# Kernel tuning notes

Measured on AMD Instinct MI355X. Metric: run time of the kernel, lower is better.

## Reference

```python
import jax, jax.numpy as jnp
import numpy as np

# Static module config (from init_kwargs)
IMG_H, IMG_W = 256, 704
NX, NY, NZ = 200, 200, 4
VOX = (0.5, 0.5, 1.5)
B, NCAM, C, HF, WF = 2, 6, 256, 64, 176
STRIDE = -(-IMG_W // WF)  # math.ceil(704/176) = 4
OUT_C = 80
BN_EPS = 1e-5


def _camera_mats():
    """Realistic lidar2image = K @ extrinsic for 6 surround cameras."""
    K = np.array([[300., 0., 352., 0.],
                  [0., 300., 128., 0.],
                  [0., 0., 1., 0.],
                  [0., 0., 0., 1.]])
    mats = []
    for a in np.linspace(0.0, 2 * np.pi, NCAM, endpoint=False):
        fwd = np.array([np.cos(a), np.sin(a), 0.0])   # camera z (forward)
        right = np.array([np.sin(a), -np.cos(a), 0.0])  # camera x
        down = np.array([0.0, 0.0, -1.0])             # camera y
        R = np.stack([right, down, fwd])
        E = np.eye(4)
        E[:3, :3] = R
        mats.append(K @ E)
    return np.stack(mats).astype(np.float32)  # [NCAM,4,4]


def setup_inputs() -> dict:
    key = jax.random.key(0)
    k1, k2, k3 = jax.random.split(key, 3)
    mlvl_feats = jax.random.normal(k1, (B, NCAM, C, HF, WF), jnp.float32)
    points = jax.random.uniform(k2, (B, NZ, NX, NY), jnp.float32)  # per-voxel weights
    lidar2image = jnp.asarray(np.tile(_camera_mats()[None], (B, 1, 1, 1)))
    img_aug_matrix = jnp.tile(jnp.eye(4, dtype=jnp.float32)[None, None], (B, NCAM, 1, 1))
    lidar_aug_matrix = jnp.tile(jnp.eye(4, dtype=jnp.float32)[None], (B, 1, 1))
    conv_w = jax.random.normal(k3, (OUT_C, C), jnp.float32) * 0.02
    conv_b = jnp.zeros((OUT_C,), jnp.float32)
    bn_gamma = jnp.ones((OUT_C,), jnp.float32)
    bn_beta = jnp.zeros((OUT_C,), jnp.float32)
    return dict(mlvl_feats=mlvl_feats, points=points, lidar2image=lidar2image,
                img_aug_matrix=img_aug_matrix, lidar_aug_matrix=lidar_aug_matrix,
                conv_w=conv_w, conv_b=conv_b, bn_gamma=bn_gamma, bn_beta=bn_beta)


def _voxel_grid():
    # get_points(): voxel-center world coordinates, [3, NX*NY*NZ]
    idx = jnp.stack(jnp.meshgrid(jnp.arange(NX), jnp.arange(NY), jnp.arange(NZ), indexing='ij'))
    vs = jnp.array(VOX, jnp.float32)
    origin = jnp.array([0.0, 0.0, -1.0], jnp.float32) - jnp.array([NX, NY, NZ], jnp.float32) / 2.0 * vs
    pts = idx.astype(jnp.float32) * vs.reshape(3, 1, 1, 1) + origin.reshape(3, 1, 1, 1)
    return pts.reshape(3, -1)


def _backproject(feat, l2i, img_aug, lidar_aug, grid):
    # feat [NCAM,C,HF,WF]; l2i/img_aug [NCAM,4,4]; lidar_aug [4,4]; grid [3,V]
    V = grid.shape[1]
    lt = lidar_aug[:3, 3]
    lr = lidar_aug[:3, :3]
    img_t = img_aug[:, :, 3]                 # [NCAM,4]
    img_r = img_aug.at[:, :, 3].set(0.0)     # zero last column
    proj = (img_r @ l2i)[:, :3, :]           # [NCAM,3,4]
    pts = lr.T @ (grid - lt[:, None])        # inverse lidar aug
    pts_h = jnp.concatenate([pts, jnp.ones((1, V), grid.dtype)], axis=0)  # [4,V]
    p2i = jnp.einsum('nij,jv->niv', proj, pts_h)  # [NCAM,3,V]
    z = p2i[:, 2]
    u = p2i[:, 0] / z + img_t[:, 0:1]
    v = p2i[:, 1] / z + img_t[:, 1:2]
    uf = jnp.round(u / STRIDE).astype(jnp.int32)
    vf = jnp.round(v / STRIDE).astype(jnp.int32)
    valid = (uf >= 0) & (vf >= 0) & (uf < WF) & (vf < HF) & (z > 0)
    uc = jnp.clip(uf, 0, WF - 1)
    vc = jnp.clip(vf, 0, HF - 1)
    vol = jnp.zeros((C, V), feat.dtype)
    # later cameras overwrite earlier ones (matches torch per-image assignment loop)
    for n in range(NCAM):
        vol = jnp.where(valid[n][None, :], feat[n][:, vc[n], uc[n]], vol)
    return vol.reshape(C, NX, NY, NZ)


def reference(mlvl_feats, points, lidar2image, img_aug_matrix, lidar_aug_matrix,
              conv_w, conv_b, bn_gamma, bn_beta):
    grid = _voxel_grid()
    volumes = jax.vmap(_backproject, in_axes=(0, 0, 0, 0, None))(
        mlvl_feats, lidar2image, img_aug_matrix, lidar_aug_matrix, grid)  # [B,C,NX,NY,NZ]
    w = jnp.transpose(points, (0, 2, 3, 1))[:, None]  # [B,1,NX,NY,NZ]
    bev = (volumes * w).sum(-1)                       # weighted z-reduction -> [B,C,NX,NY]
    y = jnp.einsum('bchw,oc->bohw', bev, conv_w) + conv_b[None, :, None, None]
    mean = y.mean((0, 2, 3), keepdims=True)
    var = y.var((0, 2, 3), keepdims=True)
    y = (y - mean) * jax.lax.rsqrt(var + BN_EPS)
    y = y * bn_gamma[None, :, None, None] + bn_beta[None, :, None, None]
    return jax.nn.relu(y)
```

## Files before the change

### kernel.cpp

```cpp
#include <hip/hip_runtime.h>

#define B_ 2
#define NCAM_ 6
#define C_ 256
#define HF_ 64
#define WF_ 176
#define NX_ 200
#define NY_ 200
#define NZ_ 4
#define V_ (NX_*NY_*NZ_)
#define HW_ (HF_*WF_)
#define OUTC_ 80
#define NPOS_ (NX_*NY_)
#define NBLK3_ 1250

typedef unsigned short u16;
typedef unsigned int   u32;
typedef __attribute__((ext_vector_type(8))) short bf16x8;
typedef __attribute__((ext_vector_type(4))) float f32x4;
typedef __attribute__((ext_vector_type(2))) unsigned int u32x2;
typedef __attribute__((ext_vector_type(4))) unsigned int u32x4;

#define WS_PROJ 0
#define WS_IMGT 144
#define WS_SCALE 256
#define WS_SHIFT 336
#define WS_WB   2048
#define WS_PF   336384
#define WS_PART 5743104
#define WS_YBF  5943104

__device__ __forceinline__ u16 f2bf(float x) {
    u32 u = __float_as_uint(x);
    u32 r = (u + 0x7fffu + ((u >> 16) & 1u)) >> 16;
    return (u16)r;
}
__device__ __forceinline__ float bf2f(u16 v) {
    return __uint_as_float(((u32)v) << 16);
}

__global__ void k0_prep(const float* __restrict__ l2i,
                        const float* __restrict__ img_aug,
                        const float* __restrict__ conv_w,
                        float* __restrict__ ws)
{
    int t = threadIdx.x;
    if (t < B_*NCAM_*12) {
        int bn = t / 12;
        int e  = t % 12;
        int i = e >> 2, j = e & 3;
        const float* A = img_aug + bn*16;
        const float* L = l2i + bn*16;
        float acc = 0.f;
        #pragma unroll
        for (int k = 0; k < 4; ++k) {
            float a = (k < 3) ? A[i*4 + k] : 0.f;
            acc = fmaf(a, L[k*4 + j], acc);
        }
        ws[WS_PROJ + t] = acc;
    }
    if (t >= 192 && t < 192 + B_*NCAM_*2) {
        int s = t - 192;
        int bn = s >> 1, i = s & 1;
        ws[WS_IMGT + s] = img_aug[bn*16 + i*4 + 3];
    }
    u32* wbp = (u32*)(ws + WS_WB);
    for (int i = t; i < 8*5*64*4; i += 256) {
        int ks = i / 1280;
        int r  = i - ks*1280;
        int u  = r >> 8;
        int r2 = r & 255;
        int l  = r2 >> 2;
        int j  = r2 & 3;
        int la = l & 15, hi = l >> 4;
        int o  = u*16 + la;
        int cb = ks*32 + ((j >> 1) << 4) + hi*4 + ((j & 1) << 1);
        wbp[i] = (u32)f2bf(conv_w[o*C_ + cb]) | ((u32)f2bf(conv_w[o*C_ + cb + 1]) << 16);
    }
}

__global__ __launch_bounds__(256, 8) void k2_mfma(const float* __restrict__ feat,
                                                  const u32* __restrict__ wbp,
                                                  u16* __restrict__ pf)
{
    __shared__ float lds[2][32][64];
    const int bn  = blockIdx.y;
    const int x   = blockIdx.x;
    const int xsw = (x & 7)*22 + (x >> 3);
    const int hw0 = xsw*64;
    const int t   = threadIdx.x;
    const int wv  = t >> 6;
    const int l   = t & 63;
    const int la  = l & 15;
    const int hi  = l >> 4;

    const float* fb = feat + (size_t)bn*C_*HW_ + hw0;

#define STAGE(buf, c0) do { \
    _Pragma("unroll") for (int i_ = 0; i_ < 2; ++i_) { \
        int r0_ = i_*16 + wv*4; \
        const float* src_ = fb + (size_t)((c0) + r0_ + (l >> 4))*HW_ + (l & 15)*4; \
        __builtin_amdgcn_global_load_lds( \
            (const __attribute__((address_space(1))) unsigned int*)src_, \
            (__attribute__((address_space(3))) unsigned int*)&lds[buf][r0_][0], \
            16, 0, 0); \
    } \
} while (0)

    f32x4 acc[5] = {};
    STAGE(0, 0);
    for (int ks = 0; ks < 8; ++ks) {
        const int cur = ks & 1;
        __syncthreads();
        if (ks < 7) STAGE(cur ^ 1, (ks+1)*32);
        const int hwl = wv*16 + la;
        union { u32 u[4]; bf16x8 v; } Bf;
        #pragma unroll
        for (int j = 0; j < 4; ++j) {
            const int cb = ((j >> 1) << 4) + hi*4 + ((j & 1) << 1);
            Bf.u[j] = (u32)f2bf(lds[cur][cb][hwl]) |
                      ((u32)f2bf(lds[cur][cb+1][hwl]) << 16);
        }
        #pragma unroll
        for (int u = 0; u < 5; ++u) {
            union { u32x4 q; bf16x8 v; } A;
            A.q = *(const u32x4*)&wbp[((ks*5 + u)*64 + l)*4];
            acc[u] = __builtin_amdgcn_mfma_f32_16x16x32_bf16(A.v, Bf.v, acc[u], 0, 0, 0);
        }
    }
#undef STAGE

    __syncthreads();
    u16* yt = (u16*)lds;
    {
        const int hwl = wv*16 + la;
        #pragma unroll
        for (int u = 0; u < 5; ++u) {
            f32x4 a = acc[u];
            u32 p0 = (u32)f2bf(a.x) | ((u32)f2bf(a.y) << 16);
            u32 p1 = (u32)f2bf(a.z) | ((u32)f2bf(a.w) << 16);
            u32x2 pk; pk.x = p0; pk.y = p1;
            *(u32x2*)&yt[hwl*80 + u*16 + hi*4] = pk;
        }
    }
    __syncthreads();
    const u32x4* src128 = (const u32x4*)yt;
    u32x4* dst128 = (u32x4*)(pf + (size_t)(bn*HW_ + hw0)*80);
    #pragma unroll
    for (int i = 0; i < 3; ++i) {
        int k = t + i*256;
        if (k < 640) dst128[k] = src128[k];
    }
}

__global__ __launch_bounds__(320) void k3_gather(const float* __restrict__ ws,
                                                 const float* __restrict__ lidar_aug,
                                                 const float* __restrict__ points,
                                                 const u16* __restrict__ pf,
                                                 const float* __restrict__ conv_b,
                                                 u16* __restrict__ ybf,
                                                 float* __restrict__ part)
{
    __shared__ int   idx_s[256];
    __shared__ float w_s[256];
    __shared__ float y_s[OUTC_][65];
    const int wlin = blockIdx.y*625 + blockIdx.x;
    const int q = NBLK3_ >> 3, r = NBLK3_ & 7;
    const int xcd = wlin & 7, iw = wlin >> 3;
    const int wg = (xcd < r) ? xcd*(q+1) + iw : r*(q+1) + (xcd - r)*q + iw;
    const int b = wg / 625;
    const int tile = wg - b*625;
    int t = threadIdx.x;
    if (t < 256) {
        int izl = t >> 6, p = t & 63;
        w_s[izl*64 + p] = points[b*V_ + izl*NPOS_ + tile*64 + p];
        int v = tile*256 + t;
        int ixy = v >> 2;
        int iz  = v & 3;
        int ix = ixy / NY_;
        int iy = ixy - ix*NY_;
        float x = ix*0.5f - 50.f;
        float y = iy*0.5f - 50.f;
        float z = iz*1.5f - 4.f;
        const float* la = lidar_aug + b*16;
        float gx = x - la[3], gy = y - la[7], gz = z - la[11];
        float px = fmaf(la[8],  gz, fmaf(la[4], gy, fmaf(la[0], gx, 0.f)));
        float py = fmaf(la[9],  gz, fmaf(la[5], gy, fmaf(la[1], gx, 0.f)));
        float pz = fmaf(la[10], gz, fmaf(la[6], gy, fmaf(la[2], gx, 0.f)));
        int best = -1;
        #pragma unroll
        for (int n = 0; n < NCAM_; ++n) {
            const float* P = ws + WS_PROJ + (b*NCAM_ + n)*12;
            float t0 = fmaf(P[3], 1.f, fmaf(P[2],  pz, fmaf(P[1], py, fmaf(P[0], px, 0.f))));
            float t1 = fmaf(P[7], 1.f, fmaf(P[6],  pz, fmaf(P[5], py, fmaf(P[4], px, 0.f))));
            float t2 = fmaf(P[11],1.f, fmaf(P[10], pz, fmaf(P[9], py, fmaf(P[8], px, 0.f))));
            float u = t0/t2 + ws[WS_IMGT + (b*NCAM_+n)*2 + 0];
            float w = t1/t2 + ws[WS_IMGT + (b*NCAM_+n)*2 + 1];
            int uf = (int)rintf(u*0.25f);
            int vf = (int)rintf(w*0.25f);
            if (uf >= 0 && vf >= 0 && uf < WF_ && vf < HF_ && t2 > 0.f)
                best = n*HW_ + vf*WF_ + uf;
        }
        idx_s[t] = best;
    }
    __syncthreads();
    int og = (t % 10)*8;
    int pg = t / 10;
    float bb0 = conv_b[og],   bb1 = conv_b[og+1], bb2 = conv_b[og+2], bb3 = conv_b[og+3];
    float bb4 = conv_b[og+4], bb5 = conv_b[og+5], bb6 = conv_b[og+6], bb7 = conv_b[og+7];
    const u16* pfb = pf + (size_t)b*(NCAM_*HW_)*80;
    #pragma unroll
    for (int i = 0; i < 2; ++i) {
        int p = pg*2 + i;
        float a0 = bb0, a1 = bb1, a2 = bb2, a3 = bb3;
        float a4 = bb4, a5 = bb5, a6 = bb6, a7 = bb7;
        #pragma unroll
        for (int iz = 0; iz < 4; ++iz) {
            int g = idx_s[p*4 + iz];
            if (g >= 0) {
                u32x4 w4 = *(const u32x4*)&pfb[(size_t)g*80 + og];
                float wgt = w_s[iz*64 + p];
                a0 = fmaf(wgt, bf2f((u16)(w4.x & 0xffff)), a0);
                a1 = fmaf(wgt, bf2f((u16)(w4.x >> 16)),    a1);
                a2 = fmaf(wgt, bf2f((u16)(w4.y & 0xffff)), a2);
                a3 = fmaf(wgt, bf2f((u16)(w4.y >> 16)),    a3);
                a4 = fmaf(wgt, bf2f((u16)(w4.z & 0xffff)), a4);
                a5 = fmaf(wgt, bf2f((u16)(w4.z >> 16)),    a5);
                a6 = fmaf(wgt, bf2f((u16)(w4.w & 0xffff)), a6);
                a7 = fmaf(wgt, bf2f((u16)(w4.w >> 16)),    a7);
            }
        }
        y_s[og][p]   = a0; y_s[og+1][p] = a1;
        y_s[og+2][p] = a2; y_s[og+3][p] = a3;
        y_s[og+4][p] = a4; y_s[og+5][p] = a5;
        y_s[og+6][p] = a6; y_s[og+7][p] = a7;
    }
    __syncthreads();
    u16* yb = ybf + (size_t)b*OUTC_*NPOS_ + tile*64;
    for (int lq = t; lq < OUTC_*32; lq += 320) {
        int oo = lq >> 5, p2 = (lq & 31) << 1;
        u32 pk = (u32)f2bf(y_s[oo][p2]) | ((u32)f2bf(y_s[oo][p2+1]) << 16);
        *(u32*)&yb[(size_t)oo*NPOS_ + p2] = pk;
    }
    int oo = t >> 2, qq = t & 3;
    float s1 = 0.f, s2 = 0.f;
    #pragma unroll
    for (int i = 0; i < 16; ++i) {
        float v = y_s[oo][qq*16 + i];
        s1 += v; s2 += v*v;
    }
    s1 += __shfl_xor(s1, 1, 4); s2 += __shfl_xor(s2, 1, 4);
    s1 += __shfl_xor(s1, 2, 4); s2 += __shfl_xor(s2, 2, 4);
    if (qq == 0) {
        int bb = b*625 + tile;
        part[oo*NBLK3_ + bb] = s1;
        part[OUTC_*NBLK3_ + oo*NBLK3_ + bb] = s2;
    }
}

__global__ __launch_bounds__(256) void k4_final(const float* __restrict__ part,
                                                const float* __restrict__ gamma,
                                                const float* __restrict__ beta,
                                                float* __restrict__ ws)
{
    int o = blockIdx.x;
    int t = threadIdx.x;
    float s1 = 0.f, s2 = 0.f;
    for (int j = t; j < NBLK3_; j += 256) {
        s1 += part[o*NBLK3_ + j];
        s2 += part[OUTC_*NBLK3_ + o*NBLK3_ + j];
    }
    __shared__ float r1[256], r2[256];
    r1[t] = s1; r2[t] = s2;
    __syncthreads();
    for (int s = 128; s > 0; s >>= 1) {
        if (t < s) { r1[t] += r1[t+s]; r2[t] += r2[t+s]; }
        __syncthreads();
    }
    if (t == 0) {
        const float invN = 1.f/(float)(B_*NPOS_);
        float mean = r1[0]*invN;
        float var  = r2[0]*invN - mean*mean;
        float inv  = rsqrtf(var + 1e-5f);
        float sc   = gamma[o]*inv;
        ws[WS_SCALE + o] = sc;
        ws[WS_SHIFT + o] = beta[o] - mean*sc;
    }
}

__global__ __launch_bounds__(256) void k5_norm(const u32* __restrict__ ybf,
                                               const float* __restrict__ ws,
                                               float* __restrict__ out)
{
    int gid = blockIdx.x*256 + threadIdx.x;
    int f = gid*8;
    if (f >= B_*OUTC_*NPOS_) return;
    int o = (f / NPOS_) % OUTC_;
    float sc = ws[WS_SCALE + o], sh = ws[WS_SHIFT + o];
    u32x4 v = *(const u32x4*)&ybf[gid*4];
    float4 r0, r1;
    r0.x = fmaxf(fmaf(bf2f((u16)(v.x & 0xffff)), sc, sh), 0.f);
    r0.y = fmaxf(fmaf(bf2f((u16)(v.x >> 16)),    sc, sh), 0.f);
    r0.z = fmaxf(fmaf(bf2f((u16)(v.y & 0xffff)), sc, sh), 0.f);
    r0.w = fmaxf(fmaf(bf2f((u16)(v.y >> 16)),    sc, sh), 0.f);
    r1.x = fmaxf(fmaf(bf2f((u16)(v.z & 0xffff)), sc, sh), 0.f);
    r1.y = fmaxf(fmaf(bf2f((u16)(v.z >> 16)),    sc, sh), 0.f);
    r1.z = fmaxf(fmaf(bf2f((u16)(v.w & 0xffff)), sc, sh), 0.f);
    r1.w = fmaxf(fmaf(bf2f((u16)(v.w >> 16)),    sc, sh), 0.f);
    *(float4*)&out[f]     = r0;
    *(float4*)&out[f + 4] = r1;
}

extern "C" void kernel_launch(void* const* d_in, const int* in_sizes, int n_in,
                              void* d_out, int out_size, void* d_ws, size_t ws_size,
                              hipStream_t stream) {
    (void)in_sizes; (void)n_in; (void)out_size; (void)ws_size;
    const float* feat      = (const float*)d_in[0];
    const float* points    = (const float*)d_in[1];
    const float* l2i       = (const float*)d_in[2];
    const float* img_aug   = (const float*)d_in[3];
    const float* lidar_aug = (const float*)d_in[4];
    const float* conv_w    = (const float*)d_in[5];
    const float* conv_b    = (const float*)d_in[6];
    const float* gamma     = (const float*)d_in[7];
    const float* beta      = (const float*)d_in[8];
    float* out = (float*)d_out;
    float* wsf = (float*)d_ws;
    u32*   wbp = (u32*)(wsf + WS_WB);
    u16*   pf  = (u16*)(wsf + WS_PF);
    float* part = wsf + WS_PART;
    u16*   ybf = (u16*)(wsf + WS_YBF);

    hipLaunchKernelGGL(k0_prep, dim3(1), dim3(256), 0, stream, l2i, img_aug, conv_w, wsf);
    hipLaunchKernelGGL(k2_mfma, dim3(HW_/64, B_*NCAM_), dim3(256), 0, stream, feat, wbp, pf);
    hipLaunchKernelGGL(k3_gather, dim3(625, B_), dim3(320), 0, stream, wsf, lidar_aug, points, pf, conv_b, ybf, part);
    hipLaunchKernelGGL(k4_final, dim3(OUTC_), dim3(256), 0, stream, part, gamma, beta, wsf);
    hipLaunchKernelGGL(k5_norm, dim3((B_*OUTC_*NPOS_/8)/256 + 1, 1), dim3(256), 0, stream, (const u32*)ybf, wsf, out);
}
```

Before: 66.67 us.

## Skip projecting feature tiles never referenced by any voxel

Adds a pass that projects every voxel into every camera and, in an occupancy bitmap, marks which 64-pixel feature tiles are the last-camera hit. The MFMA channel-projection kernel then exits early for tiles no voxel uses, avoiding their feature loads and matrix work. This costs an extra kernel launch and the per-voxel projection maths, and it relies on the flag computation matching the gather kernel's indexing exactly.

```diff
diff --git a/kernel.cpp b/kernel.cpp
--- a/kernel.cpp
+++ b/kernel.cpp
@@ -25,6 +25,7 @@
 #define WS_IMGT 144
 #define WS_SCALE 256
 #define WS_SHIFT 336
+#define WS_FLG  1024
 #define WS_WB   2048
 #define WS_PF   336384
 #define WS_PART 5743104
@@ -64,6 +65,8 @@
         int bn = s >> 1, i = s & 1;
         ws[WS_IMGT + s] = img_aug[bn*16 + i*4 + 3];
     }
+    u32* flags = (u32*)(ws + WS_FLG);
+    if (t < 66) flags[t] = 0;
     u32* wbp = (u32*)(ws + WS_WB);
     for (int i = t; i < 8*5*64*4; i += 256) {
         int ks = i / 1280;
@@ -79,8 +82,52 @@
     }
 }
 
+__global__ __launch_bounds__(256) void k1_flags(const float* __restrict__ ws,
+                                                const float* __restrict__ lidar_aug,
+                                                u32* __restrict__ flags)
+{
+    __shared__ u32 fl[33];
+    const int wg = blockIdx.x;
+    const int b = wg / 625;
+    const int tile = wg - b*625;
+    const int t = threadIdx.x;
+    if (t < 33) fl[t] = 0;
+    __syncthreads();
+    int v = tile*256 + t;
+    int ixy = v >> 2;
+    int iz  = v & 3;
+    int ix = ixy / NY_;
+    int iy = ixy - ix*NY_;
+    float x = ix*0.5f - 50.f;
+    float y = iy*0.5f - 50.f;
+    float z = iz*1.5f - 4.f;
+    const float* la = lidar_aug + b*16;
+    float gx = x - la[3], gy = y - la[7], gz = z - la[11];
+    float px = fmaf(la[8],  gz, fmaf(la[4], gy, fmaf(la[0], gx, 0.f)));
+    float py = fmaf(la[9],  gz, fmaf(la[5], gy, fmaf(la[1], gx, 0.f)));
+    float pz = fmaf(la[10], gz, fmaf(la[6], gy, fmaf(la[2], gx, 0.f)));
+    int best = -1;
+    #pragma unroll
+    for (int n = 0; n < NCAM_; ++n) {
+        const float* P = ws + WS_PROJ + (b*NCAM_ + n)*12;
+        float t0 = fmaf(P[3], 1.f, fmaf(P[2],  pz, fmaf(P[1], py, fmaf(P[0], px, 0.f))));
+        float t1 = fmaf(P[7], 1.f, fmaf(P[6],  pz, fmaf(P[5], py, fmaf(P[4], px, 0.f))));
+        float t2 = fmaf(P[11],1.f, fmaf(P[10], pz, fmaf(P[9], py, fmaf(P[8], px, 0.f))));
+        float u = t0/t2 + ws[WS_IMGT + (b*NCAM_+n)*2 + 0];
+        float w = t1/t2 + ws[WS_IMGT + (b*NCAM_+n)*2 + 1];
+        int uf = (int)rintf(u*0.25f);
+        int vf = (int)rintf(w*0.25f);
+        if (uf >= 0 && vf >= 0 && uf < WF_ && vf < HF_ && t2 > 0.f)
+            best = n*HW_ + vf*WF_ + uf;
+    }
+    if (best >= 0) atomicOr(&fl[best >> 11], 1u << ((best >> 6) & 31));
+    __syncthreads();
+    if (t < 33 && fl[t]) atomicOr(&flags[b*33 + t], fl[t]);
+}
+
 __global__ __launch_bounds__(256, 8) void k2_mfma(const float* __restrict__ feat,
                                                   const u32* __restrict__ wbp,
+                                                  const u32* __restrict__ flags,
                                                   u16* __restrict__ pf)
 {
     __shared__ float lds[2][32][64];
@@ -88,6 +135,10 @@
     const int x   = blockIdx.x;
     const int xsw = (x & 7)*22 + (x >> 3);
     const int hw0 = xsw*64;
+    const int b_ = bn / 6, n_ = bn - b_*6;
+    const int gt = n_*176 + xsw;
+    if (!(flags[b_*33 + (gt >> 5)] & (1u << (gt & 31)))) return;
+
     const int t   = threadIdx.x;
     const int wv  = t >> 6;
     const int l   = t & 63;
@@ -326,13 +377,15 @@
     const float* beta      = (const float*)d_in[8];
     float* out = (float*)d_out;
     float* wsf = (float*)d_ws;
+    u32*   flags = (u32*)(wsf + WS_FLG);
     u32*   wbp = (u32*)(wsf + WS_WB);
     u16*   pf  = (u16*)(wsf + WS_PF);
     float* part = wsf + WS_PART;
     u16*   ybf = (u16*)(wsf + WS_YBF);
 
     hipLaunchKernelGGL(k0_prep, dim3(1), dim3(256), 0, stream, l2i, img_aug, conv_w, wsf);
-    hipLaunchKernelGGL(k2_mfma, dim3(HW_/64, B_*NCAM_), dim3(256), 0, stream, feat, wbp, pf);
+    hipLaunchKernelGGL(k1_flags, dim3(NBLK3_), dim3(256), 0, stream, wsf, lidar_aug, flags);
+    hipLaunchKernelGGL(k2_mfma, dim3(HW_/64, B_*NCAM_), dim3(256), 0, stream, feat, wbp, flags, pf);
     hipLaunchKernelGGL(k3_gather, dim3(625, B_), dim3(320), 0, stream, wsf, lidar_aug, points, pf, conv_b, ybf, part);
     hipLaunchKernelGGL(k4_final, dim3(OUTC_), dim3(256), 0, stream, part, gamma, beta, wsf);
     hipLaunchKernelGGL(k5_norm, dim3((B_*OUTC_*NPOS_/8)/256 + 1, 1), dim3(256), 0, stream, (const u32*)ybf, wsf, out);
```

Result: slower. 77.52 us (+16.3%).
